# Kernel optimization log

Hardware: AMD Instinct MI355X
Metric: run time of the kernel (lower is better)

The kernel has to match this reference:

```python
import jax, jax.numpy as jnp
import numpy as np

N_EMBEDDINGS = 1024
EMBEDDING_DIM = 256
DECAY = 0.99
EPSILON = 1e-05


def setup_inputs() -> dict:
    key = jax.random.key(0)
    k1, k2, k3 = jax.random.split(key, 3)
    inputs = jax.random.normal(k1, (16, 64, 64, EMBEDDING_DIM), dtype=jnp.float32)
    codebook = jax.random.normal(k2, (N_EMBEDDINGS, EMBEDDING_DIM), dtype=jnp.float32)
    ema_w = jax.random.normal(k3, (N_EMBEDDINGS, EMBEDDING_DIM), dtype=jnp.float32)
    ema_cluster_size = jnp.zeros((N_EMBEDDINGS,), dtype=jnp.float32)
    return {"inputs": inputs, "codebook": codebook, "ema_w": ema_w,
            "ema_cluster_size": ema_cluster_size}


def reference(inputs, codebook, ema_w, ema_cluster_size):
    input_shape = inputs.shape
    flat = inputs.reshape(-1, EMBEDDING_DIM)  # [N, D]
    # Squared Euclidean pairwise distances: [N, K]
    dists = (jnp.sum(flat * flat, axis=1, keepdims=True)
             + jnp.sum(codebook * codebook, axis=1)[None, :]
             - 2.0 * flat @ codebook.T)
    idx = jnp.argmin(dists, axis=1)  # [N]
    encodings = jax.nn.one_hot(idx, N_EMBEDDINGS, dtype=flat.dtype)  # [N, K]
    quantized = (encodings @ codebook).reshape(input_shape)
    # EMA updates (training mode)
    cs = ema_cluster_size * DECAY + (1.0 - DECAY) * jnp.sum(encodings, axis=0)
    n = jnp.sum(cs)
    cs = (cs + EPSILON) / (n + cs * EPSILON) * n  # faithful to original expression
    dw = encodings.T @ flat  # [K, D] scatter-accumulate via matmul
    new_ema_w = ema_w * DECAY + (1.0 - DECAY) * dw
    new_codebook = new_ema_w / cs[:, None]
    return quantized, encodings, cs, new_ema_w, new_codebook
```

## Files before the change

### kernel.cpp

```cpp
#include <hip/hip_runtime.h>

#define N_ROWS 65536
#define D 256
#define K 1024
#define DECAYF 0.99f
#define OMDF 0.01f
#define EPSF 1e-5f

typedef _Float16 f16;
typedef _Float16 f16x8 __attribute__((ext_vector_type(8)));
typedef float f32x16 __attribute__((ext_vector_type(16)));
typedef float f32x4 __attribute__((ext_vector_type(4)));

__global__ __launch_bounds__(256) void prep_kernel(const float* __restrict__ cb,
                                                   float* __restrict__ cnorm,
                                                   char* __restrict__ wsB,
                                                   float* __restrict__ dw,
                                                   float* __restrict__ counts) {
    const int tid = threadIdx.x;
    const int bid = blockIdx.x;
    const int g = bid * 256 + tid;
    *reinterpret_cast<float4*>(dw + (size_t)g * 4) = make_float4(0.f, 0.f, 0.f, 0.f);
    if (g < K) counts[g] = 0.f;
    {
        const int row = bid * 4 + (tid >> 6);
        const int lane = tid & 63;
        const float4 v = *reinterpret_cast<const float4*>(cb + (size_t)row * D + lane * 4);
        float s = v.x * v.x + v.y * v.y + v.z * v.z + v.w * v.w;
        #pragma unroll
        for (int m = 32; m; m >>= 1) s += __shfl_xor(s, m);
        if (lane == 0) cnorm[row] = s;
    }
    {
        const int l31 = g & 31;
        const int h   = (g >> 5) & 1;
        const int cfg = (g >> 6) & 7;
        const int v   = (g >> 9) & 1;
        const int ks  = (g >> 10) & 3;
        const int dk  = (g >> 12) & 3;
        const int ct  = (g >> 14) & 3;
        const int code = ct * 256 + cfg * 32 + l31;
        const int dim0 = dk * 64 + ks * 16 + h * 8;
        const float* src = cb + (size_t)code * D + dim0;
        f16 out[8];
        #pragma unroll
        for (int e = 0; e < 8; ++e) {
            const float f = src[e];
            const f16 hi = (f16)f;
            out[e] = v ? (f16)(f - (float)hi) : hi;
        }
        *reinterpret_cast<f16x8*>(wsB + (size_t)g * 16) = *reinterpret_cast<f16x8*>(out);
    }
}

__device__ __forceinline__ void load_b(const char* __restrict__ wsB, int ct, int t,
                                       int cfg0, int lane16,
                                       f16x8& b00, f16x8& b10, f16x8& b01, f16x8& b11) {
    const int dk = t >> 2, ks = t & 3;
    const int sbase = (((ct * 4 + dk) * 4 + ks) * 2) * 8;
    b00 = *reinterpret_cast<const f16x8*>(wsB + (size_t)(sbase + cfg0 + 0) * 1024 + lane16);
    b10 = *reinterpret_cast<const f16x8*>(wsB + (size_t)(sbase + cfg0 + 1) * 1024 + lane16);
    b01 = *reinterpret_cast<const f16x8*>(wsB + (size_t)(sbase + 8 + cfg0 + 0) * 1024 + lane16);
    b11 = *reinterpret_cast<const f16x8*>(wsB + (size_t)(sbase + 8 + cfg0 + 1) * 1024 + lane16);
}

__global__ __launch_bounds__(256, 2) void argmin_mfma_kernel(
        const float* __restrict__ x, const char* __restrict__ wsB,
        const float* __restrict__ cnorm, int* __restrict__ idx_out,
        float* __restrict__ counts) {
    __shared__ char smem[67584];
    const int tid = threadIdx.x;
    const int cw = tid >> 6;
    const int lane = tid & 63;
    const int l31 = lane & 31;
    const int h = lane >> 5;
    const int n0 = blockIdx.x * 64;

    {
        const int s_row = tid >> 2;
        const int c4 = tid & 3;
        const f32x4* src = reinterpret_cast<const f32x4*>(
            x + (size_t)(n0 + s_row) * D + c4 * 64);
        char* rowbase = smem + s_row * 1024;
        const int sw = s_row & 7;
        #pragma unroll
        for (int j = 0; j < 8; ++j) {
            const f32x4 f0 = __builtin_nontemporal_load(src + j * 2);
            const f32x4 f1 = __builtin_nontemporal_load(src + j * 2 + 1);
            float f[8] = {f0[0], f0[1], f0[2], f0[3], f1[0], f1[1], f1[2], f1[3]};
            f16 hi8[8], lo8[8];
            #pragma unroll
            for (int e = 0; e < 8; ++e) {
                hi8[e] = (f16)f[e];
                lo8[e] = (f16)(f[e] - (float)hi8[e]);
            }
            const int ph = (c4 * 8 + j) ^ sw;
            *reinterpret_cast<f16x8*>(rowbase + ph * 16)       = *reinterpret_cast<f16x8*>(hi8);
            *reinterpret_cast<f16x8*>(rowbase + 512 + ph * 16) = *reinterpret_cast<f16x8*>(lo8);
        }
    }
    __syncthreads();

    float bestv[2][16];
    int besti[2][16];
    #pragma unroll
    for (int rf = 0; rf < 2; ++rf)
        #pragma unroll
        for (int r = 0; r < 16; ++r) { bestv[rf][r] = 3.4e38f; besti[rf][r] = 0; }

    const int lane16 = lane * 16;
    const int arow0 = l31;
    const int arow1 = 32 + l31;
    char* abase0 = smem + arow0 * 1024;
    char* abase1 = smem + arow1 * 1024;
    const int asw0 = arow0 & 7;
    const int asw1 = arow1 & 7;
    const int cfg0 = cw * 2;

    f16x8 pb00, pb10, pb01, pb11;
    load_b(wsB, 0, 0, cfg0, lane16, pb00, pb10, pb01, pb11);

    #pragma unroll 1
    for (int ct = 0; ct < 4; ++ct) {
        f32x16 acc[2][2];
        #pragma unroll
        for (int rf = 0; rf < 2; ++rf)
            #pragma unroll
            for (int cf = 0; cf < 2; ++cf)
                #pragma unroll
                for (int r = 0; r < 16; ++r) acc[rf][cf][r] = 0.f;

        #pragma unroll
        for (int t = 0; t < 16; ++t) {
            const f16x8 B00 = pb00, B10 = pb10, B01 = pb01, B11 = pb11;
            if (!(ct == 3 && t == 15)) {
                const int nct = (t == 15) ? ct + 1 : ct;
                const int ntt = (t == 15) ? 0 : t + 1;
                load_b(wsB, nct, ntt, cfg0, lane16, pb00, pb10, pb01, pb11);
            }
            const int g = t * 2 + h;
            const f16x8 Ah0 = *reinterpret_cast<const f16x8*>(abase0 + ((g ^ asw0) * 16));
            const f16x8 Al0 = *reinterpret_cast<const f16x8*>(abase0 + 512 + ((g ^ asw0) * 16));
            const f16x8 Ah1 = *reinterpret_cast<const f16x8*>(abase1 + ((g ^ asw1) * 16));
            const f16x8 Al1 = *reinterpret_cast<const f16x8*>(abase1 + 512 + ((g ^ asw1) * 16));
            acc[0][0] = __builtin_amdgcn_mfma_f32_32x32x16_f16(Ah0, B00, acc[0][0], 0, 0, 0);
            acc[0][0] = __builtin_amdgcn_mfma_f32_32x32x16_f16(Ah0, B01, acc[0][0], 0, 0, 0);
            acc[0][0] = __builtin_amdgcn_mfma_f32_32x32x16_f16(Al0, B00, acc[0][0], 0, 0, 0);
            acc[0][1] = __builtin_amdgcn_mfma_f32_32x32x16_f16(Ah0, B10, acc[0][1], 0, 0, 0);
            acc[0][1] = __builtin_amdgcn_mfma_f32_32x32x16_f16(Ah0, B11, acc[0][1], 0, 0, 0);
            acc[0][1] = __builtin_amdgcn_mfma_f32_32x32x16_f16(Al0, B10, acc[0][1], 0, 0, 0);
            acc[1][0] = __builtin_amdgcn_mfma_f32_32x32x16_f16(Ah1, B00, acc[1][0], 0, 0, 0);
            acc[1][0] = __builtin_amdgcn_mfma_f32_32x32x16_f16(Ah1, B01, acc[1][0], 0, 0, 0);
            acc[1][0] = __builtin_amdgcn_mfma_f32_32x32x16_f16(Al1, B00, acc[1][0], 0, 0, 0);
            acc[1][1] = __builtin_amdgcn_mfma_f32_32x32x16_f16(Ah1, B10, acc[1][1], 0, 0, 0);
            acc[1][1] = __builtin_amdgcn_mfma_f32_32x32x16_f16(Ah1, B11, acc[1][1], 0, 0, 0);
            acc[1][1] = __builtin_amdgcn_mfma_f32_32x32x16_f16(Al1, B10, acc[1][1], 0, 0, 0);
        }
        const int code0 = ct * 256 + cw * 64 + l31;
        const int code1 = code0 + 32;
        const float cn0 = cnorm[code0];
        const float cn1 = cnorm[code1];
        #pragma unroll
        for (int rf = 0; rf < 2; ++rf)
            #pragma unroll
            for (int r = 0; r < 16; ++r) {
                const float d0 = cn0 - 2.f * acc[rf][0][r];
                const float d1 = cn1 - 2.f * acc[rf][1][r];
                float dv = d0; int db = code0;
                if (d1 < dv) { dv = d1; db = code1; }
                if (dv < bestv[rf][r]) { bestv[rf][r] = dv; besti[rf][r] = db; }
            }
    }
    #pragma unroll
    for (int rf = 0; rf < 2; ++rf)
        #pragma unroll
        for (int r = 0; r < 16; ++r) {
            float v = bestv[rf][r];
            int b = besti[rf][r];
            #pragma unroll
            for (int m = 16; m; m >>= 1) {
                const float ov = __shfl_xor(v, m);
                const int ob = __shfl_xor(b, m);
                if (ov < v || (ov == v && ob < b)) { v = ov; b = ob; }
            }
            bestv[rf][r] = v; besti[rf][r] = b;
        }
    __syncthreads();
    float* Sv = reinterpret_cast<float*>(smem + 65536);
    int*   Si = reinterpret_cast<int*>(smem + 66560);
    if (l31 == 0) {
        #pragma unroll
        for (int rf = 0; rf < 2; ++rf)
            #pragma unroll
            for (int r = 0; r < 16; ++r) {
                const int row = rf * 32 + (r & 3) + 8 * (r >> 2) + 4 * h;
                Sv[cw * 64 + row] = bestv[rf][r];
                Si[cw * 64 + row] = besti[rf][r];
            }
    }
    __syncthreads();
    if (tid < 64) {
        float v = Sv[tid];
        int b = Si[tid];
        #pragma unroll
        for (int w = 1; w < 4; ++w) {
            const float ov = Sv[w * 64 + tid];
            const int ob = Si[w * 64 + tid];
            if (ov < v || (ov == v && ob < b)) { v = ov; b = ob; }
        }
        idx_out[n0 + tid] = b;
        atomicAdd(&counts[b], 1.0f);
    }
}

__global__ __launch_bounds__(256) void quant_kernel(const float* __restrict__ cb,
                                                    const int* __restrict__ idx,
                                                    float* __restrict__ quant) {
    const int n = blockIdx.x * 4 + (threadIdx.x >> 6);
    const int lane = threadIdx.x & 63;
    const int i = idx[n];
    const f32x4 c = *reinterpret_cast<const f32x4*>(cb + (size_t)i * D + lane * 4);
    __builtin_nontemporal_store(c, reinterpret_cast<f32x4*>(quant + (size_t)n * D + lane * 4));
}

__global__ __launch_bounds__(256) void enc_kernel(const int* __restrict__ idx,
                                                  float* __restrict__ enc) {
    const int total = N_ROWS * (K / 4);
    for (int g = blockIdx.x * blockDim.x + threadIdx.x; g < total;
         g += gridDim.x * blockDim.x) {
        const int n = g >> 8;
        const int k0 = (g & 255) * 4;
        const int i = idx[n];
        f32x4 v;
        v[0] = (k0 == i) ? 1.f : 0.f;
        v[1] = (k0 + 1 == i) ? 1.f : 0.f;
        v[2] = (k0 + 2 == i) ? 1.f : 0.f;
        v[3] = (k0 + 3 == i) ? 1.f : 0.f;
        __builtin_nontemporal_store(v, reinterpret_cast<f32x4*>(enc + (size_t)g * 4));
    }
}

__global__ __launch_bounds__(1024) void cs_scan_kernel(const float* __restrict__ ema_cs,
                                                       const float* __restrict__ counts,
                                                       float* __restrict__ cs_out,
                                                       int* __restrict__ cursor) {
    __shared__ float wsum[16];
    __shared__ int wisum[16];
    __shared__ float n_sh;
    const int k = threadIdx.x;
    const int wid = k >> 6;
    const int lane = k & 63;
    const float cnt = counts[k];
    const float c = ema_cs[k] * DECAYF + OMDF * cnt;
    const int ic = (int)cnt;
    int v = ic;
    #pragma unroll
    for (int d = 1; d < 64; d <<= 1) {
        const int t = __shfl_up(v, d);
        if (lane >= d) v += t;
    }
    float s = c;
    #pragma unroll
    for (int m = 32; m; m >>= 1) s += __shfl_xor(s, m);
    if (lane == 63) wisum[wid] = v;
    if (lane == 0) wsum[wid] = s;
    __syncthreads();
    if (k == 0) {
        float n = 0.f;
        for (int w = 0; w < 16; ++w) n += wsum[w];
        n_sh = n;
    }
    if (wid == 0 && lane < 16) {
        int wv = wisum[lane];
        #pragma unroll
        for (int d = 1; d < 16; d <<= 1) {
            const int t = __shfl_up(wv, d);
            if (lane >= d) wv += t;
        }
        wisum[lane] = wv;
    }
    __syncthreads();
    const float n = n_sh;
    cs_out[k] = (c + EPSF) / (n + c * EPSF) * n;
    const int wbase = (wid == 0) ? 0 : wisum[wid - 1];
    cursor[k] = wbase + v - ic;
}

__global__ __launch_bounds__(256) void scatter_kernel(const int* __restrict__ idx,
                                                      int* __restrict__ cursor,
                                                      int* __restrict__ rowlist,
                                                      int* __restrict__ codelist) {
    __shared__ int hist[1024];
    const int tid = threadIdx.x;
    #pragma unroll
    for (int j = 0; j < 4; ++j) hist[tid + j * 256] = 0;
    __syncthreads();
    const int n = blockIdx.x * 256 + tid;
    const int i = idx[n];
    atomicAdd(&hist[i], 1);
    __syncthreads();
    #pragma unroll
    for (int j = 0; j < 4; ++j) {
        const int k = tid + j * 256;
        const int c = hist[k];
        hist[k] = (c > 0) ? atomicAdd(&cursor[k], c) : 0;
    }
    __syncthreads();
    const int pos = atomicAdd(&hist[i], 1);
    rowlist[pos] = n;
    codelist[pos] = i;
}

__global__ __launch_bounds__(256) void chunk_sum_kernel(const float* __restrict__ x,
                                                        const int* __restrict__ rowlist,
                                                        const int* __restrict__ codelist,
                                                        float* __restrict__ dw) {
    const int wave = threadIdx.x >> 6;
    const int lane = threadIdx.x & 63;
    const int p0 = blockIdx.x * 32 + wave * 8;
    int rows[8], codes[8];
    #pragma unroll
    for (int j = 0; j < 8; ++j) {
        rows[j] = rowlist[p0 + j];
        codes[j] = codelist[p0 + j];
    }
    f32x4 v[8];
    #pragma unroll
    for (int j = 0; j < 8; ++j)
        v[j] = __builtin_nontemporal_load(
            reinterpret_cast<const f32x4*>(x + (size_t)rows[j] * D + lane * 4));
    f32x4 s = v[0];
    int cur = codes[0];
    #pragma unroll
    for (int j = 1; j < 8; ++j) {
        if (codes[j] != cur) {
            float* dst = dw + (size_t)cur * D + lane * 4;
            atomicAdd(dst + 0, s[0]); atomicAdd(dst + 1, s[1]);
            atomicAdd(dst + 2, s[2]); atomicAdd(dst + 3, s[3]);
            cur = codes[j];
            s = v[j];
        } else {
            s[0] += v[j][0]; s[1] += v[j][1]; s[2] += v[j][2]; s[3] += v[j][3];
        }
    }
    float* dst = dw + (size_t)cur * D + lane * 4;
    atomicAdd(dst + 0, s[0]); atomicAdd(dst + 1, s[1]);
    atomicAdd(dst + 2, s[2]); atomicAdd(dst + 3, s[3]);
}

__global__ __launch_bounds__(256) void ema_kernel(const float* __restrict__ ema_w,
                                                  const float* __restrict__ dw,
                                                  const float* __restrict__ cs,
                                                  float* __restrict__ w_out,
                                                  float* __restrict__ cb_out) {
    const int e4 = blockIdx.x * blockDim.x + threadIdx.x;
    const int k = e4 >> 6;
    const float csk = cs[k];
    const float4 w = *reinterpret_cast<const float4*>(ema_w + (size_t)e4 * 4);
    const float4 d = *reinterpret_cast<const float4*>(dw + (size_t)e4 * 4);
    float4 nw, nc;
    nw.x = w.x * DECAYF + OMDF * d.x;
    nw.y = w.y * DECAYF + OMDF * d.y;
    nw.z = w.z * DECAYF + OMDF * d.z;
    nw.w = w.w * DECAYF + OMDF * d.w;
    nc.x = nw.x / csk; nc.y = nw.y / csk; nc.z = nw.z / csk; nc.w = nw.w / csk;
    *reinterpret_cast<float4*>(w_out + (size_t)e4 * 4) = nw;
    *reinterpret_cast<float4*>(cb_out + (size_t)e4 * 4) = nc;
}

extern "C" void kernel_launch(void* const* d_in, const int* in_sizes, int n_in,
                              void* d_out, int out_size, void* d_ws, size_t ws_size,
                              hipStream_t stream) {
    (void)in_sizes; (void)n_in; (void)out_size; (void)ws_size;
    const float* x      = (const float*)d_in[0];
    const float* cb     = (const float*)d_in[1];
    const float* ema_w  = (const float*)d_in[2];
    const float* ema_cs = (const float*)d_in[3];

    float* out    = (float*)d_out;
    float* quant  = out;
    float* enc    = quant + 16777216;
    float* cs_out = enc + 67108864;
    float* w_out  = cs_out + 1024;
    float* cb_out = w_out + 262144;

    float* ws       = (float*)d_ws;
    float* counts   = ws;
    float* dw       = ws + 1024;
    float* cnorm    = ws + 263168;
    int*   cursor   = (int*)(ws + 264192);
    int*   idx      = (int*)(ws + 265216);
    int*   rowlist  = (int*)(ws + 330752);
    int*   codelist = (int*)(ws + 396288);
    char*  wsB      = (char*)(ws + 461824);

    prep_kernel<<<256, 256, 0, stream>>>(cb, cnorm, wsB, dw, counts);
    argmin_mfma_kernel<<<N_ROWS / 64, 256, 0, stream>>>(x, wsB, cnorm, idx, counts);
    quant_kernel<<<N_ROWS / 4, 256, 0, stream>>>(cb, idx, quant);
    enc_kernel<<<2048, 256, 0, stream>>>(idx, enc);
    cs_scan_kernel<<<1, 1024, 0, stream>>>(ema_cs, counts, cs_out, cursor);
    scatter_kernel<<<N_ROWS / 256, 256, 0, stream>>>(idx, cursor, rowlist, codelist);
    chunk_sum_kernel<<<2048, 256, 0, stream>>>(x, rowlist, codelist, dw);
    ema_kernel<<<65536 / 256, 256, 0, stream>>>(ema_w, dw, cs_out, w_out, cb_out);
}
```

Measured before the change: 398.7 us.

## Retile argmin GEMM to 256-row blocks with LDS-staged codebook K-slices

The argmin kernel now processes 256 rows per block with 8 waves (2 row-waves by 4 code-waves). It streams the input and codebook in 32-dim K-slices through LDS, instead of holding a full 64-row A tile in LDS and reading B directly from global memory. This raises B reuse across more rows and cuts global codebook traffic per row. In exchange, A is re-read from global for each code tile, with a serpentine order that reuses the last slice. It also adds two barriers per slice, removes B register prefetching, and does per-code-tile reductions into LDS.

```diff
diff --git a/kernel.cpp b/kernel.cpp
--- a/kernel.cpp
+++ b/kernel.cpp
@@ -53,159 +53,138 @@
     }
 }
 
-__device__ __forceinline__ void load_b(const char* __restrict__ wsB, int ct, int t,
-                                       int cfg0, int lane16,
-                                       f16x8& b00, f16x8& b10, f16x8& b01, f16x8& b11) {
-    const int dk = t >> 2, ks = t & 3;
-    const int sbase = (((ct * 4 + dk) * 4 + ks) * 2) * 8;
-    b00 = *reinterpret_cast<const f16x8*>(wsB + (size_t)(sbase + cfg0 + 0) * 1024 + lane16);
-    b10 = *reinterpret_cast<const f16x8*>(wsB + (size_t)(sbase + cfg0 + 1) * 1024 + lane16);
-    b01 = *reinterpret_cast<const f16x8*>(wsB + (size_t)(sbase + 8 + cfg0 + 0) * 1024 + lane16);
-    b11 = *reinterpret_cast<const f16x8*>(wsB + (size_t)(sbase + 8 + cfg0 + 1) * 1024 + lane16);
-}
-
-__global__ __launch_bounds__(256, 2) void argmin_mfma_kernel(
+__global__ __launch_bounds__(512, 2) void argmin_mfma_kernel(
         const float* __restrict__ x, const char* __restrict__ wsB,
         const float* __restrict__ cnorm, int* __restrict__ idx_out,
         float* __restrict__ counts) {
-    __shared__ char smem[67584];
+    __shared__ char smem[73728];
+    char* Alds = smem;
+    char* Blds = smem + 32768;
+    float* Sv = reinterpret_cast<float*>(smem + 65536);
+    int*   Si = reinterpret_cast<int*>(smem + 69632);
     const int tid = threadIdx.x;
-    const int cw = tid >> 6;
+    const int wave = tid >> 6;
     const int lane = tid & 63;
     const int l31 = lane & 31;
     const int h = lane >> 5;
-    const int n0 = blockIdx.x * 64;
-
-    {
-        const int s_row = tid >> 2;
-        const int c4 = tid & 3;
-        const f32x4* src = reinterpret_cast<const f32x4*>(
-            x + (size_t)(n0 + s_row) * D + c4 * 64);
-        char* rowbase = smem + s_row * 1024;
-        const int sw = s_row & 7;
-        #pragma unroll
-        for (int j = 0; j < 8; ++j) {
-            const f32x4 f0 = __builtin_nontemporal_load(src + j * 2);
-            const f32x4 f1 = __builtin_nontemporal_load(src + j * 2 + 1);
-            float f[8] = {f0[0], f0[1], f0[2], f0[3], f1[0], f1[1], f1[2], f1[3]};
-            f16 hi8[8], lo8[8];
-            #pragma unroll
-            for (int e = 0; e < 8; ++e) {
-                hi8[e] = (f16)f[e];
-                lo8[e] = (f16)(f[e] - (float)hi8[e]);
-            }
-            const int ph = (c4 * 8 + j) ^ sw;
-            *reinterpret_cast<f16x8*>(rowbase + ph * 16)       = *reinterpret_cast<f16x8*>(hi8);
-            *reinterpret_cast<f16x8*>(rowbase + 512 + ph * 16) = *reinterpret_cast<f16x8*>(lo8);
-        }
-    }
-    __syncthreads();
-
-    float bestv[2][16];
-    int besti[2][16];
-    #pragma unroll
-    for (int rf = 0; rf < 2; ++rf)
-        #pragma unroll
-        for (int r = 0; r < 16; ++r) { bestv[rf][r] = 3.4e38f; besti[rf][r] = 0; }
-
-    const int lane16 = lane * 16;
-    const int arow0 = l31;
-    const int arow1 = 32 + l31;
-    char* abase0 = smem + arow0 * 1024;
-    char* abase1 = smem + arow1 * 1024;
-    const int asw0 = arow0 & 7;
-    const int asw1 = arow1 & 7;
-    const int cfg0 = cw * 2;
-
-    f16x8 pb00, pb10, pb01, pb11;
-    load_b(wsB, 0, 0, cfg0, lane16, pb00, pb10, pb01, pb11);
+    const int rw = wave >> 2;
+    const int cw = wave & 3;
+    const int n0 = blockIdx.x * 256;
+
+    Sv[tid] = 3.4e38f; Sv[tid + 512] = 3.4e38f;
+    Si[tid] = 0; Si[tid + 512] = 0;
+
+    const int s_row = tid >> 1;
+    const int c16 = tid & 1;
+    const int ssw = s_row & 7;
+    char* s_rowbase = Alds + s_row * 128;
+
+    const int arow[4] = { rw * 128 + l31, rw * 128 + 32 + l31,
+                          rw * 128 + 64 + l31, rw * 128 + 96 + l31 };
 
     #pragma unroll 1
     for (int ct = 0; ct < 4; ++ct) {
-        f32x16 acc[2][2];
-        #pragma unroll
-        for (int rf = 0; rf < 2; ++rf)
+        f32x16 acc[4][2];
+        #pragma unroll
+        for (int rf = 0; rf < 4; ++rf)
             #pragma unroll
             for (int cf = 0; cf < 2; ++cf)
                 #pragma unroll
                 for (int r = 0; r < 16; ++r) acc[rf][cf][r] = 0.f;
 
-        #pragma unroll
-        for (int t = 0; t < 16; ++t) {
-            const f16x8 B00 = pb00, B10 = pb10, B01 = pb01, B11 = pb11;
-            if (!(ct == 3 && t == 15)) {
-                const int nct = (t == 15) ? ct + 1 : ct;
-                const int ntt = (t == 15) ? 0 : t + 1;
-                load_b(wsB, nct, ntt, cfg0, lane16, pb00, pb10, pb01, pb11);
+        #pragma unroll 1
+        for (int p = 0; p < 8; ++p) {
+            const int dk2 = (ct & 1) ? (7 - p) : p;
+            __syncthreads();
+            if (!(ct > 0 && p == 0)) {
+                const f32x4* src = reinterpret_cast<const f32x4*>(
+                    x + (size_t)(n0 + s_row) * D + dk2 * 32 + c16 * 16);
+                const f32x4 a0 = __builtin_nontemporal_load(src + 0);
+                const f32x4 a1 = __builtin_nontemporal_load(src + 1);
+                const f32x4 a2 = __builtin_nontemporal_load(src + 2);
+                const f32x4 a3 = __builtin_nontemporal_load(src + 3);
+                float f[16] = {a0[0],a0[1],a0[2],a0[3], a1[0],a1[1],a1[2],a1[3],
+                               a2[0],a2[1],a2[2],a2[3], a3[0],a3[1],a3[2],a3[3]};
+                f16 hi8[16], lo8[16];
+                #pragma unroll
+                for (int e = 0; e < 16; ++e) {
+                    hi8[e] = (f16)f[e];
+                    lo8[e] = (f16)(f[e] - (float)hi8[e]);
+                }
+                #pragma unroll
+                for (int hp = 0; hp < 2; ++hp) {
+                    const int ghi = (c16 * 2 + hp) ^ ssw;
+                    const int glo = (4 + c16 * 2 + hp) ^ ssw;
+                    *reinterpret_cast<f16x8*>(s_rowbase + ghi * 16) = *reinterpret_cast<f16x8*>(&hi8[hp * 8]);
+                    *reinterpret_cast<f16x8*>(s_rowbase + glo * 16) = *reinterpret_cast<f16x8*>(&lo8[hp * 8]);
+                }
             }
-            const int g = t * 2 + h;
-            const f16x8 Ah0 = *reinterpret_cast<const f16x8*>(abase0 + ((g ^ asw0) * 16));
-            const f16x8 Al0 = *reinterpret_cast<const f16x8*>(abase0 + 512 + ((g ^ asw0) * 16));
-            const f16x8 Ah1 = *reinterpret_cast<const f16x8*>(abase1 + ((g ^ asw1) * 16));
-            const f16x8 Al1 = *reinterpret_cast<const f16x8*>(abase1 + 512 + ((g ^ asw1) * 16));
-            acc[0][0] = __builtin_amdgcn_mfma_f32_32x32x16_f16(Ah0, B00, acc[0][0], 0, 0, 0);
-            acc[0][0] = __builtin_amdgcn_mfma_f32_32x32x16_f16(Ah0, B01, acc[0][0], 0, 0, 0);
-            acc[0][0] = __builtin_amdgcn_mfma_f32_32x32x16_f16(Al0, B00, acc[0][0], 0, 0, 0);
-            acc[0][1] = __builtin_amdgcn_mfma_f32_32x32x16_f16(Ah0, B10, acc[0][1], 0, 0, 0);
-            acc[0][1] = __builtin_amdgcn_mfma_f32_32x32x16_f16(Ah0, B11, acc[0][1], 0, 0, 0);
-            acc[0][1] = __builtin_amdgcn_mfma_f32_32x32x16_f16(Al0, B10, acc[0][1], 0, 0, 0);
-            acc[1][0] = __builtin_amdgcn_mfma_f32_32x32x16_f16(Ah1, B00, acc[1][0], 0, 0, 0);
-            acc[1][0] = __builtin_amdgcn_mfma_f32_32x32x16_f16(Ah1, B01, acc[1][0], 0, 0, 0);
-            acc[1][0] = __builtin_amdgcn_mfma_f32_32x32x16_f16(Al1, B00, acc[1][0], 0, 0, 0);
-            acc[1][1] = __builtin_amdgcn_mfma_f32_32x32x16_f16(Ah1, B10, acc[1][1], 0, 0, 0);
-            acc[1][1] = __builtin_amdgcn_mfma_f32_32x32x16_f16(Ah1, B11, acc[1][1], 0, 0, 0);
-            acc[1][1] = __builtin_amdgcn_mfma_f32_32x32x16_f16(Al1, B10, acc[1][1], 0, 0, 0);
-        }
-        const int code0 = ct * 256 + cw * 64 + l31;
-        const int code1 = code0 + 32;
-        const float cn0 = cnorm[code0];
-        const float cn1 = cnorm[code1];
-        #pragma unroll
-        for (int rf = 0; rf < 2; ++rf)
+            {
+                const int4* gsrc = reinterpret_cast<const int4*>(wsB + (size_t)(ct * 8 + dk2) * 32768);
+                int4* ldst = reinterpret_cast<int4*>(Blds);
+                #pragma unroll
+                for (int i = 0; i < 4; ++i) ldst[tid + i * 512] = gsrc[tid + i * 512];
+            }
+            __syncthreads();
+            #pragma unroll
+            for (int ks2 = 0; ks2 < 2; ++ks2) {
+                const int g = ks2 * 2 + h;
+                f16x8 Ah[4], Al[4];
+                #pragma unroll
+                for (int rf = 0; rf < 4; ++rf) {
+                    char* ab = Alds + arow[rf] * 128;
+                    const int asw = arow[rf] & 7;
+                    Ah[rf] = *reinterpret_cast<const f16x8*>(ab + ((g ^ asw) * 16));
+                    Al[rf] = *reinterpret_cast<const f16x8*>(ab + (((4 + g) ^ asw) * 16));
+                }
+                #pragma unroll
+                for (int cf = 0; cf < 2; ++cf) {
+                    const int cfg = cw * 2 + cf;
+                    const f16x8 Bh = *reinterpret_cast<const f16x8*>(Blds + (ks2 * 16 + cfg) * 1024 + lane * 16);
+                    const f16x8 Bl = *reinterpret_cast<const f16x8*>(Blds + (ks2 * 16 + 8 + cfg) * 1024 + lane * 16);
+                    #pragma unroll
+                    for (int rf = 0; rf < 4; ++rf) {
+                        acc[rf][cf] = __builtin_amdgcn_mfma_f32_32x32x16_f16(Ah[rf], Bh, acc[rf][cf], 0, 0, 0);
+                        acc[rf][cf] = __builtin_amdgcn_mfma_f32_32x32x16_f16(Ah[rf], Bl, acc[rf][cf], 0, 0, 0);
+                        acc[rf][cf] = __builtin_amdgcn_mfma_f32_32x32x16_f16(Al[rf], Bh, acc[rf][cf], 0, 0, 0);
+                    }
+                }
+            }
+        }
+        const int codebase = ct * 256 + cw * 64;
+        const float cn0 = cnorm[codebase + l31];
+        const float cn1 = cnorm[codebase + 32 + l31];
+        #pragma unroll
+        for (int rf = 0; rf < 4; ++rf) {
             #pragma unroll
             for (int r = 0; r < 16; ++r) {
                 const float d0 = cn0 - 2.f * acc[rf][0][r];
                 const float d1 = cn1 - 2.f * acc[rf][1][r];
-                float dv = d0; int db = code0;
-                if (d1 < dv) { dv = d1; db = code1; }
-                if (dv < bestv[rf][r]) { bestv[rf][r] = dv; besti[rf][r] = db; }
+                float v = d0; int b = codebase + l31;
+                if (d1 < v) { v = d1; b = codebase + 32 + l31; }
+                #pragma unroll
+                for (int m = 16; m; m >>= 1) {
+                    const float ov = __shfl_xor(v, m);
+                    const int ob = __shfl_xor(b, m);
+                    if (ov < v || (ov == v && ob < b)) { v = ov; b = ob; }
+                }
+                if (l31 == 0) {
+                    const int row = rw * 128 + rf * 32 + (r & 3) + 8 * (r >> 2) + 4 * h;
+                    const int slot = cw * 256 + row;
+                    const float pv = Sv[slot]; const int pb = Si[slot];
+                    if (v < pv || (v == pv && b < pb)) { Sv[slot] = v; Si[slot] = b; }
+                }
             }
-    }
-    #pragma unroll
-    for (int rf = 0; rf < 2; ++rf)
-        #pragma unroll
-        for (int r = 0; r < 16; ++r) {
-            float v = bestv[rf][r];
-            int b = besti[rf][r];
-            #pragma unroll
-            for (int m = 16; m; m >>= 1) {
-                const float ov = __shfl_xor(v, m);
-                const int ob = __shfl_xor(b, m);
-                if (ov < v || (ov == v && ob < b)) { v = ov; b = ob; }
-            }
-            bestv[rf][r] = v; besti[rf][r] = b;
-        }
-    __syncthreads();
-    float* Sv = reinterpret_cast<float*>(smem + 65536);
-    int*   Si = reinterpret_cast<int*>(smem + 66560);
-    if (l31 == 0) {
-        #pragma unroll
-        for (int rf = 0; rf < 2; ++rf)
-            #pragma unroll
-            for (int r = 0; r < 16; ++r) {
-                const int row = rf * 32 + (r & 3) + 8 * (r >> 2) + 4 * h;
-                Sv[cw * 64 + row] = bestv[rf][r];
-                Si[cw * 64 + row] = besti[rf][r];
-            }
-    }
-    __syncthreads();
-    if (tid < 64) {
+        }
+    }
+    __syncthreads();
+    if (tid < 256) {
         float v = Sv[tid];
         int b = Si[tid];
         #pragma unroll
         for (int w = 1; w < 4; ++w) {
-            const float ov = Sv[w * 64 + tid];
-            const int ob = Si[w * 64 + tid];
+            const float ov = Sv[w * 256 + tid];
+            const int ob = Si[w * 256 + tid];
             if (ov < v || (ov == v && ob < b)) { v = ov; b = ob; }
         }
         idx_out[n0 + tid] = b;
@@ -395,7 +374,7 @@
     char*  wsB      = (char*)(ws + 461824);
 
     prep_kernel<<<256, 256, 0, stream>>>(cb, cnorm, wsB, dw, counts);
-    argmin_mfma_kernel<<<N_ROWS / 64, 256, 0, stream>>>(x, wsB, cnorm, idx, counts);
+    argmin_mfma_kernel<<<N_ROWS / 256, 512, 0, stream>>>(x, wsB, cnorm, idx, counts);
     quant_kernel<<<N_ROWS / 4, 256, 0, stream>>>(cb, idx, quant);
     enc_kernel<<<2048, 256, 0, stream>>>(idx, enc);
     cs_scan_kernel<<<1, 1024, 0, stream>>>(ema_cs, counts, cs_out, cursor);
```

Result: slower. 549.7 us (+37.8%).
